# Kernel tuning notes

Measured on AMD Instinct MI355X. Metric: run time of the kernel, lower is better.

## Reference

```python
import jax, jax.numpy as jnp
import numpy as np

N = 50000        # total nodes across batch
K = 16           # max neighbors per node (padded with index 0)
E = 800000       # directed edges / messages
B = 1024         # molecules
MAXM = 48        # max nodes per molecule (padded with index 0)
FEATURE_FDIM = 9
ALL_FDIM = 10    # feature_dist_graph (9) + reshaped rij distance (1)
H = 64           # hidden_dim
NUM_ITERS = 2
NEG_INF = -1e9


def setup_inputs() -> dict:
    key = jax.random.key(0)
    ks = jax.random.split(key, 16)
    s = 1.0 / np.sqrt(H)
    return {
        "target_features": jax.random.normal(ks[0], (N, FEATURE_FDIM), jnp.float32),
        "feature_dist_graph": jax.random.normal(ks[1], (E, ALL_FDIM - 1), jnp.float32),
        "rij_dist_pairs": jax.random.uniform(ks[2], (E,), jnp.float32),
        "start_end_env": jax.random.randint(ks[3], (N, K), 0, N + 1),
        "b_scope": jax.random.randint(ks[4], (N, K), 0, E),
        "l_scope": jax.random.randint(ks[5], (B, MAXM), 0, N + 1),
        "scope_update": jax.random.randint(ks[6], (E,), 0, N + 1),
        "scope_update_lig": jax.random.randint(ks[7], (E,), 0, N + 1),
        "W_emb": jax.random.uniform(ks[8], (FEATURE_FDIM, H), jnp.float32, 0.1, 0.9),
        "b_emb": jnp.zeros((H,), jnp.float32),
        "W_dist": jax.random.uniform(ks[9], (ALL_FDIM, H), jnp.float32, 0.1, 0.9),
        "b_dist": jnp.zeros((H,), jnp.float32),
        "W_gat": jax.random.normal(ks[10], (H, H), jnp.float32) * s,
        "Wm_gat": jax.random.normal(ks[11], (H, H), jnp.float32) * s,
        "a_gat": jax.random.normal(ks[12], (2 * H,), jnp.float32) * s,
    }


def reference(target_features, feature_dist_graph, rij_dist_pairs,
              start_end_env, b_scope, l_scope, scope_update, scope_update_lig,
              W_emb, b_emb, W_dist, b_dist, W_gat, Wm_gat, a_gat):
    # node embedding over origin features
    h = target_features @ W_emb + b_emb                        # [N, H]
    # edge message embedding over pair features + distance
    msg_in = jnp.concatenate([feature_dist_graph, rij_dist_pairs[:, None]], axis=1)
    message = msg_in @ W_dist + b_dist                         # [E, H]
    # prepend zero pad row (index 0 = padding for ragged gathers)
    hp = jnp.concatenate([jnp.zeros((1, H), h.dtype), h], axis=0)  # [N+1, H]
    pad_mask = (start_end_env == 0)                            # [N, K]
    upd_mask = (scope_update_lig > 0).astype(h.dtype)[:, None]  # [E, 1]
    for _ in range(NUM_ITERS):
        nb = hp[start_end_env]                                 # [N, K, H] gather neighbors
        mg = message[b_scope]                                  # [N, K, H] gather messages
        Wn = nb @ W_gat                                        # [N, K, H]
        Wm = mg @ Wm_gat                                       # [N, K, H]
        # GAT attention logits: leaky_relu(a^T [Wn || Wm])
        logits = jax.nn.leaky_relu(
            jnp.einsum('nkh,h->nk', Wn, a_gat[:H]) +
            jnp.einsum('nkh,h->nk', Wm, a_gat[H:]), 0.2)       # [N, K]
        logits = jnp.where(pad_mask, NEG_INF, logits)
        alpha = jax.nn.softmax(logits, axis=1)                 # [N, K]
        new_h = jax.nn.elu(jnp.einsum('nk,nkh->nh', alpha, Wn + Wm))  # [N, H]
        hp = jnp.concatenate([jnp.zeros((1, H), new_h.dtype), new_h], axis=0)
        # scatter updated node features back into edge messages
        message = hp[scope_update] * upd_mask                  # [E, H]
    cmp_enc = hp[l_scope]                                      # [B, MAXM, H]
    return cmp_enc.sum(axis=1)                                 # [B, H]
```

## Files before the change

kernel.cpp:

```cpp
#include <hip/hip_runtime.h>
#include <hip/hip_bf16.h>

#define N_NODES 50000
#define K_NB 16
#define E_EDGES 800000
#define B_MOL 1024
#define MAXM_M 48
#define FDIM 9
#define ADIM 10
#define H 64
#define NEG_INF_F (-1e9f)
#define NODE_BLOCKS 12500
#define EDGE_BLOCKS 3125

__device__ inline float readlane_f(float v, int l) {
    return __int_as_float(__builtin_amdgcn_readlane(__float_as_int(v), l));
}
__device__ inline int readlane_i(int v, int l) {
    return __builtin_amdgcn_readlane(v, l);
}
__device__ inline float bf2f(unsigned u) {
    return __uint_as_float(u << 16);
}
__device__ inline unsigned short f2bf(float f) {
    unsigned x = __float_as_uint(f);
    return (unsigned short)((x + 0x7fffu + ((x >> 16) & 1u)) >> 16);
}

#define GLOAD_U16(dst, voff, sbase) \
    asm volatile("global_load_ushort %0, %1, %2" : "=v"(dst) : "v"(voff), "s"(sbase))
#define GLOAD_F32(dst, voff, sbase) \
    asm volatile("global_load_dword %0, %1, %2" : "=v"(dst) : "v"(voff), "s"(sbase))

__global__ __launch_bounds__(256) void k_fold(
    const float* __restrict__ W_emb, const float* __restrict__ b_emb,
    const float* __restrict__ W_dist, const float* __restrict__ b_dist,
    const float* __restrict__ W_gat, const float* __restrict__ Wm_gat,
    const float* __restrict__ a_gat,
    float* __restrict__ W2, float* __restrict__ c2,
    float* __restrict__ W3, float* __restrict__ c3,
    float* __restrict__ wa, float* __restrict__ ca)
{
    int tid = blockIdx.x * 256 + threadIdx.x;
    if (tid < 640) {
        int j = tid >> 6, h = tid & 63;
        float acc = 0.f;
        for (int t = 0; t < H; ++t) acc += W_dist[j * H + t] * Wm_gat[t * H + h];
        W2[tid] = acc;
    } else if (tid < 704) {
        int h = tid - 640;
        float acc = 0.f;
        for (int t = 0; t < H; ++t) acc += b_dist[t] * Wm_gat[t * H + h];
        c2[h] = acc;
    } else if (tid < 1280) {
        int q = tid - 704, j = q >> 6, h = q & 63;
        float acc = 0.f;
        for (int t = 0; t < H; ++t) acc += W_emb[j * H + t] * W_gat[t * H + h];
        W3[q] = acc;
    } else if (tid < 1344) {
        int h = tid - 1280;
        float acc = 0.f;
        for (int t = 0; t < H; ++t) acc += b_emb[t] * W_gat[t * H + h];
        c3[h] = acc;
    } else if (tid < 1408) {
        int lane = tid - 1344;
        float v = 0.f;
        for (int h = 0; h < H; ++h) v += Wm_gat[lane * H + h] * a_gat[H + h];
        float acc = 0.f;
        for (int t = 0; t < H; ++t) {
            float vt = readlane_f(v, t);
            if (lane < ADIM)       acc += W_dist[lane * H + t] * vt;
            else if (lane == ADIM) acc += b_dist[t] * vt;
        }
        if (lane < ADIM)       wa[lane] = acc;
        else if (lane == ADIM) ca[0] = acc;
    }
}

__global__ __launch_bounds__(256) void k_pre(
    const float* __restrict__ tf, const float* __restrict__ fdg,
    const float* __restrict__ rij,
    const int* __restrict__ su, const int* __restrict__ sul,
    const float* __restrict__ W3, const float* __restrict__ c3,
    const float* __restrict__ wa, const float* __restrict__ ca,
    const float* __restrict__ a_gat,
    unsigned short* __restrict__ WGh16, float* __restrict__ t1,
    unsigned short* __restrict__ emsg, int* __restrict__ sue)
{
    int bid = blockIdx.x;
    if (bid < NODE_BLOCKS) {
        int tid = bid * 256 + threadIdx.x;
        int n = tid >> 6, h = tid & 63;
        if (tid < 64) { WGh16[tid] = 0; if (tid == 0) t1[0] = 0.f; }
        float acc = c3[h];
#pragma unroll
        for (int j = 0; j < FDIM; ++j) acc += tf[n * FDIM + j] * W3[j * H + h];
        WGh16[(size_t)(n + 1) * H + h] = f2bf(acc);
        float tv = acc * a_gat[h];
#pragma unroll
        for (int o = 32; o > 0; o >>= 1) tv += __shfl_xor(tv, o, 64);
        if (h == 0) t1[n + 1] = tv;
    } else {
        int e = (bid - NODE_BLOCKS) * 256 + threadIdx.x;
        float f[ADIM];
#pragma unroll
        for (int j = 0; j < FDIM; ++j) f[j] = fdg[(size_t)e * FDIM + j];
        f[FDIM] = rij[e];
        float acc = ca[0];
#pragma unroll
        for (int j = 0; j < ADIM; ++j) acc += f[j] * wa[j];
        unsigned rec[8];
#pragma unroll
        for (int j = 0; j < 5; ++j)
            rec[j] = (unsigned)f2bf(f[2 * j]) | ((unsigned)f2bf(f[2 * j + 1]) << 16);
        rec[5] = __float_as_uint(acc);
        rec[6] = 0; rec[7] = 0;
        uint4* dst = (uint4*)(emsg + (size_t)e * 16);
        dst[0] = make_uint4(rec[0], rec[1], rec[2], rec[3]);
        dst[1] = make_uint4(rec[4], rec[5], rec[6], rec[7]);
        sue[e] = (sul[e] > 0) ? su[e] : 0;
    }
}

template <int ITER>
__global__ __launch_bounds__(256) void k_gat(
    const int* __restrict__ sse, const int* __restrict__ bsc,
    const unsigned short* __restrict__ WGh16, const float* __restrict__ t1,
    const unsigned short* __restrict__ emsg,
    const float* __restrict__ W2, const float* __restrict__ c2,
    const int* __restrict__ sue, const float* __restrict__ t2,
    const unsigned short* __restrict__ WhWm16,
    float* __restrict__ hp_out)
{
    int wave = threadIdx.x >> 6;
    int lane = threadIdx.x & 63;
    int n = blockIdx.x * 4 + wave;
    if (n == 0) hp_out[lane] = 0.f;
    if (n >= N_NODES) return;

    int kidx = 0, ke = 0, ksu = 0;
    float lg = NEG_INF_F;
    if (lane < K_NB) {
        kidx = sse[n * K_NB + lane];
        ke   = bsc[n * K_NB + lane];
        float g2;
        if (ITER == 1) {
            g2 = __uint_as_float(*(const unsigned*)(emsg + (size_t)ke * 16 + 10));
        } else {
            ksu = sue[ke];
            g2 = t2[ksu];
        }
        float p = t1[kidx] + g2;
        p = (p > 0.f) ? p : 0.2f * p;
        lg = (kidx == 0) ? NEG_INF_F : p;
    }

    unsigned wn_u[K_NB], wm_u[K_NB];
    int off  = lane * 2;
    int offm = (lane & 15) * 2;
#pragma unroll
    for (int k = 0; k < K_NB; ++k) {
        const unsigned short* pk = WGh16 + (size_t)readlane_i(kidx, k) * H;
        GLOAD_U16(wn_u[k], off, pk);
    }
#pragma unroll
    for (int k = 0; k < K_NB; ++k) {
        if (ITER == 1) {
            const unsigned short* pe = emsg + (size_t)readlane_i(ke, k) * 16;
            GLOAD_U16(wm_u[k], offm, pe);
        } else {
            const unsigned short* ps = WhWm16 + (size_t)readlane_i(ksu, k) * H;
            GLOAD_U16(wm_u[k], off, ps);
        }
    }

    float m = lg;
#pragma unroll
    for (int o = 8; o > 0; o >>= 1) m = fmaxf(m, __shfl_xor(m, o, 64));
    float ex = __expf(lg - m);
    float s = ex;
#pragma unroll
    for (int o = 8; o > 0; o >>= 1) s += __shfl_xor(s, o, 64);
    float alpha = ex / s;

    asm volatile("s_waitcnt vmcnt(0)"
        : "+v"(wn_u[0]), "+v"(wn_u[1]), "+v"(wn_u[2]), "+v"(wn_u[3]),
          "+v"(wn_u[4]), "+v"(wn_u[5]), "+v"(wn_u[6]), "+v"(wn_u[7]),
          "+v"(wn_u[8]), "+v"(wn_u[9]), "+v"(wn_u[10]), "+v"(wn_u[11]),
          "+v"(wn_u[12]), "+v"(wn_u[13]), "+v"(wn_u[14]), "+v"(wn_u[15]));
    asm volatile(""
        : "+v"(wm_u[0]), "+v"(wm_u[1]), "+v"(wm_u[2]), "+v"(wm_u[3]),
          "+v"(wm_u[4]), "+v"(wm_u[5]), "+v"(wm_u[6]), "+v"(wm_u[7]),
          "+v"(wm_u[8]), "+v"(wm_u[9]), "+v"(wm_u[10]), "+v"(wm_u[11]),
          "+v"(wm_u[12]), "+v"(wm_u[13]), "+v"(wm_u[14]), "+v"(wm_u[15]));

    float acc = 0.f;
    float fr = 0.f;
#pragma unroll
    for (int k = 0; k < K_NB; ++k) {
        float ak = readlane_f(alpha, k);
        if (ITER == 1) {
            acc += ak * bf2f(wn_u[k]);
            fr  += ak * bf2f(wm_u[k]);
        } else {
            acc += ak * (bf2f(wn_u[k]) + bf2f(wm_u[k]));
        }
    }
    if (ITER == 1) {
        float wmacc = c2[lane];
#pragma unroll
        for (int j = 0; j < ADIM; ++j)
            wmacc += readlane_f(fr, j) * W2[j * H + lane];
        acc += wmacc;
    }
    float o = (acc > 0.f) ? acc : expm1f(acc);
    hp_out[(size_t)(n + 1) * H + lane] = o;
}

__global__ __launch_bounds__(256) void k_gemm2(
    const float* __restrict__ hp,
    const float* __restrict__ W_gat, const float* __restrict__ Wm_gat,
    const float* __restrict__ a_gat,
    unsigned short* __restrict__ WGh16, unsigned short* __restrict__ WhWm16,
    float* __restrict__ t1, float* __restrict__ t2)
{
    int lane = threadIdx.x & 63;
    float wg[H], wm[H];
#pragma unroll
    for (int j = 0; j < H; ++j) {
        wg[j] = W_gat[j * H + lane];
        wm[j] = Wm_gat[j * H + lane];
    }
    float a1 = a_gat[lane], a2 = a_gat[H + lane];
    int row = blockIdx.x * 4 + (threadIdx.x >> 6);
    int stride = gridDim.x * 4;
    for (; row <= N_NODES; row += stride) {
        float hv = hp[(size_t)row * H + lane];
        float a = 0.f, b = 0.f;
#pragma unroll
        for (int j = 0; j < H; ++j) {
            float hj = readlane_f(hv, j);
            a += hj * wg[j];
            b += hj * wm[j];
        }
        WGh16[(size_t)row * H + lane]  = f2bf(a);
        WhWm16[(size_t)row * H + lane] = f2bf(b);
        float ta = a * a1, tb = b * a2;
#pragma unroll
        for (int o = 32; o > 0; o >>= 1) {
            ta += __shfl_xor(ta, o, 64);
            tb += __shfl_xor(tb, o, 64);
        }
        if (lane == 0) { t1[row] = ta; t2[row] = tb; }
    }
}

__global__ __launch_bounds__(256) void k_out(
    const int* __restrict__ l_scope, const float* __restrict__ hp,
    float* __restrict__ out)
{
    int wave = threadIdx.x >> 6;
    int lane = threadIdx.x & 63;
    int b = blockIdx.x * 4 + wave;
    if (b >= B_MOL) return;
    int idx48 = (lane < MAXM_M) ? l_scope[b * MAXM_M + lane] : 0;
    float v[MAXM_M];
    int off = lane * 4;
#pragma unroll
    for (int m = 0; m < MAXM_M; ++m) {
        const float* pm = hp + (size_t)readlane_i(idx48, m) * H;
        GLOAD_F32(v[m], off, pm);
    }
    asm volatile("s_waitcnt vmcnt(0)"
        : "+v"(v[0]), "+v"(v[1]), "+v"(v[2]), "+v"(v[3]),
          "+v"(v[4]), "+v"(v[5]), "+v"(v[6]), "+v"(v[7]),
          "+v"(v[8]), "+v"(v[9]), "+v"(v[10]), "+v"(v[11]),
          "+v"(v[12]), "+v"(v[13]), "+v"(v[14]), "+v"(v[15]));
    asm volatile(""
        : "+v"(v[16]), "+v"(v[17]), "+v"(v[18]), "+v"(v[19]),
          "+v"(v[20]), "+v"(v[21]), "+v"(v[22]), "+v"(v[23]),
          "+v"(v[24]), "+v"(v[25]), "+v"(v[26]), "+v"(v[27]),
          "+v"(v[28]), "+v"(v[29]), "+v"(v[30]), "+v"(v[31]));
    asm volatile(""
        : "+v"(v[32]), "+v"(v[33]), "+v"(v[34]), "+v"(v[35]),
          "+v"(v[36]), "+v"(v[37]), "+v"(v[38]), "+v"(v[39]),
          "+v"(v[40]), "+v"(v[41]), "+v"(v[42]), "+v"(v[43]),
          "+v"(v[44]), "+v"(v[45]), "+v"(v[46]), "+v"(v[47]));
    float acc = 0.f;
#pragma unroll
    for (int m = 0; m < MAXM_M; ++m) acc += v[m];
    out[b * H + lane] = acc;
}

extern "C" void kernel_launch(void* const* d_in, const int* in_sizes, int n_in,
                              void* d_out, int out_size, void* d_ws, size_t ws_size,
                              hipStream_t stream)
{
    const float* tf     = (const float*)d_in[0];
    const float* fdg    = (const float*)d_in[1];
    const float* rij    = (const float*)d_in[2];
    const int*   sse    = (const int*)d_in[3];
    const int*   bsc    = (const int*)d_in[4];
    const int*   lsc    = (const int*)d_in[5];
    const int*   su     = (const int*)d_in[6];
    const int*   sul    = (const int*)d_in[7];
    const float* W_emb  = (const float*)d_in[8];
    const float* b_emb  = (const float*)d_in[9];
    const float* W_dist = (const float*)d_in[10];
    const float* b_dist = (const float*)d_in[11];
    const float* W_gat  = (const float*)d_in[12];
    const float* Wm_gat = (const float*)d_in[13];
    const float* a_gat  = (const float*)d_in[14];
    float* out = (float*)d_out;

    char* base = (char*)d_ws;
    size_t off = 0;
    auto alloc = [&](size_t bytes) {
        char* p = base + off;
        off = (off + bytes + 255) & ~(size_t)255;
        return p;
    };
    float* W2   = (float*)alloc(640 * 4);
    float* c2   = (float*)alloc(64 * 4);
    float* W3   = (float*)alloc(576 * 4);
    float* c3   = (float*)alloc(64 * 4);
    float* wa   = (float*)alloc(16 * 4);
    float* ca   = (float*)alloc(16 * 4);
    float* t1   = (float*)alloc((size_t)(N_NODES + 1) * 4);
    float* t2   = (float*)alloc((size_t)(N_NODES + 1) * 4);
    int*   sue  = (int*)alloc((size_t)E_EDGES * 4);
    unsigned short* WGh16  = (unsigned short*)alloc((size_t)(N_NODES + 1) * H * 2);
    unsigned short* WhWm16 = (unsigned short*)alloc((size_t)(N_NODES + 1) * H * 2);
    float* hp2  = (float*)alloc((size_t)(N_NODES + 1) * H * 4);
    char*  big  = alloc((size_t)E_EDGES * 32);
    unsigned short* emsg = (unsigned short*)big;
    float* hp3  = (float*)big;

    k_fold<<<dim3(6), dim3(256), 0, stream>>>(W_emb, b_emb, W_dist, b_dist,
                                              W_gat, Wm_gat, a_gat,
                                              W2, c2, W3, c3, wa, ca);

    k_pre<<<dim3(NODE_BLOCKS + EDGE_BLOCKS), dim3(256), 0, stream>>>(
        tf, fdg, rij, su, sul, W3, c3, wa, ca, a_gat, WGh16, t1, emsg, sue);

    dim3 gat_grid((N_NODES + 3) / 4);
    k_gat<1><<<gat_grid, dim3(256), 0, stream>>>(
        sse, bsc, WGh16, t1, emsg, W2, c2, sue, t2, WhWm16, hp2);

    k_gemm2<<<dim3(1024), dim3(256), 0, stream>>>(
        hp2, W_gat, Wm_gat, a_gat, WGh16, WhWm16, t1, t2);

    k_gat<2><<<gat_grid, dim3(256), 0, stream>>>(
        sse, bsc, WGh16, t1, emsg, W2, c2, sue, t2, WhWm16, hp3);

    k_out<<<dim3(B_MOL / 4), dim3(256), 0, stream>>>(lsc, hp3, out);
}
```

Baseline: 234.2 us.

## Aggregate raw features before projection and fold the second GEMM into gather kernels

```diff
diff --git a/kernel.cpp b/kernel.cpp
--- a/kernel.cpp
+++ b/kernel.cpp
@@ -10,7 +10,7 @@
 #define ADIM 10
 #define H 64
 #define NEG_INF_F (-1e9f)
-#define NODE_BLOCKS 12500
+#define PRE_NODE_BLOCKS 196
 #define EDGE_BLOCKS 3125
 
 __device__ inline float readlane_f(float v, int l) {
@@ -31,6 +31,19 @@
     asm volatile("global_load_ushort %0, %1, %2" : "=v"(dst) : "v"(voff), "s"(sbase))
 #define GLOAD_F32(dst, voff, sbase) \
     asm volatile("global_load_dword %0, %1, %2" : "=v"(dst) : "v"(voff), "s"(sbase))
+
+#define DRAIN16(a) \
+    asm volatile("s_waitcnt vmcnt(0)" \
+        : "+v"(a[0]), "+v"(a[1]), "+v"(a[2]), "+v"(a[3]), \
+          "+v"(a[4]), "+v"(a[5]), "+v"(a[6]), "+v"(a[7]), \
+          "+v"(a[8]), "+v"(a[9]), "+v"(a[10]), "+v"(a[11]), \
+          "+v"(a[12]), "+v"(a[13]), "+v"(a[14]), "+v"(a[15]))
+#define HOLD16(a) \
+    asm volatile("" \
+        : "+v"(a[0]), "+v"(a[1]), "+v"(a[2]), "+v"(a[3]), \
+          "+v"(a[4]), "+v"(a[5]), "+v"(a[6]), "+v"(a[7]), \
+          "+v"(a[8]), "+v"(a[9]), "+v"(a[10]), "+v"(a[11]), \
+          "+v"(a[12]), "+v"(a[13]), "+v"(a[14]), "+v"(a[15]))
 
 __global__ __launch_bounds__(256) void k_fold(
     const float* __restrict__ W_emb, const float* __restrict__ b_emb,
@@ -39,41 +52,60 @@
     const float* __restrict__ a_gat,
     float* __restrict__ W2, float* __restrict__ c2,
     float* __restrict__ W3, float* __restrict__ c3,
-    float* __restrict__ wa, float* __restrict__ ca)
-{
-    int tid = blockIdx.x * 256 + threadIdx.x;
-    if (tid < 640) {
-        int j = tid >> 6, h = tid & 63;
-        float acc = 0.f;
-        for (int t = 0; t < H; ++t) acc += W_dist[j * H + t] * Wm_gat[t * H + h];
-        W2[tid] = acc;
-    } else if (tid < 704) {
-        int h = tid - 640;
+    float* __restrict__ wa, float* __restrict__ ca,
+    float* __restrict__ va, float* __restrict__ vb,
+    float* __restrict__ wv9, float* __restrict__ cv)
+{
+    __shared__ float s_va[64], s_vb[64];
+    int tid = threadIdx.x;
+    int h = tid & 63, g = tid >> 6;
+    if (g == 0) {
+        float acc = 0.f;
+        for (int t = 0; t < H; ++t) acc += W_gat[h * H + t] * a_gat[t];
+        s_va[h] = acc; va[h] = acc;
+    } else if (g == 1) {
+        float acc = 0.f;
+        for (int t = 0; t < H; ++t) acc += Wm_gat[h * H + t] * a_gat[H + t];
+        s_vb[h] = acc; vb[h] = acc;
+    } else if (g == 2) {
         float acc = 0.f;
         for (int t = 0; t < H; ++t) acc += b_dist[t] * Wm_gat[t * H + h];
         c2[h] = acc;
-    } else if (tid < 1280) {
-        int q = tid - 704, j = q >> 6, h = q & 63;
-        float acc = 0.f;
-        for (int t = 0; t < H; ++t) acc += W_emb[j * H + t] * W_gat[t * H + h];
-        W3[q] = acc;
-    } else if (tid < 1344) {
-        int h = tid - 1280;
+    } else {
         float acc = 0.f;
         for (int t = 0; t < H; ++t) acc += b_emb[t] * W_gat[t * H + h];
         c3[h] = acc;
-    } else if (tid < 1408) {
-        int lane = tid - 1344;
-        float v = 0.f;
-        for (int h = 0; h < H; ++h) v += Wm_gat[lane * H + h] * a_gat[H + h];
-        float acc = 0.f;
-        for (int t = 0; t < H; ++t) {
-            float vt = readlane_f(v, t);
-            if (lane < ADIM)       acc += W_dist[lane * H + t] * vt;
-            else if (lane == ADIM) acc += b_dist[t] * vt;
-        }
-        if (lane < ADIM)       wa[lane] = acc;
-        else if (lane == ADIM) ca[0] = acc;
+    }
+    __syncthreads();
+    for (int q = tid; q < 640; q += 256) {
+        int j = q >> 6, hh = q & 63;
+        float acc = 0.f;
+        for (int t = 0; t < H; ++t) acc += W_dist[j * H + t] * Wm_gat[t * H + hh];
+        W2[q] = acc;
+    }
+    for (int q = tid; q < 576; q += 256) {
+        int j = q >> 6, hh = q & 63;
+        float acc = 0.f;
+        for (int t = 0; t < H; ++t) acc += W_emb[j * H + t] * W_gat[t * H + hh];
+        W3[q] = acc;
+    }
+    if (tid < ADIM) {
+        float acc = 0.f;
+        for (int t = 0; t < H; ++t) acc += W_dist[tid * H + t] * s_vb[t];
+        wa[tid] = acc;
+    } else if (tid == ADIM) {
+        float acc = 0.f;
+        for (int t = 0; t < H; ++t) acc += b_dist[t] * s_vb[t];
+        ca[0] = acc;
+    } else if (tid >= 16 && tid < 16 + FDIM) {
+        int j = tid - 16;
+        float acc = 0.f;
+        for (int t = 0; t < H; ++t) acc += W_emb[j * H + t] * s_va[t];
+        wv9[j] = acc;
+    } else if (tid == 31) {
+        float acc = 0.f;
+        for (int t = 0; t < H; ++t) acc += b_emb[t] * s_va[t];
+        cv[0] = acc;
     }
 }
 
@@ -81,27 +113,39 @@
     const float* __restrict__ tf, const float* __restrict__ fdg,
     const float* __restrict__ rij,
     const int* __restrict__ su, const int* __restrict__ sul,
-    const float* __restrict__ W3, const float* __restrict__ c3,
     const float* __restrict__ wa, const float* __restrict__ ca,
-    const float* __restrict__ a_gat,
-    unsigned short* __restrict__ WGh16, float* __restrict__ t1,
+    const float* __restrict__ wv9, const float* __restrict__ cv,
+    float* __restrict__ t1A, unsigned short* __restrict__ tfp,
     unsigned short* __restrict__ emsg, int* __restrict__ sue)
 {
     int bid = blockIdx.x;
-    if (bid < NODE_BLOCKS) {
-        int tid = bid * 256 + threadIdx.x;
-        int n = tid >> 6, h = tid & 63;
-        if (tid < 64) { WGh16[tid] = 0; if (tid == 0) t1[0] = 0.f; }
-        float acc = c3[h];
-#pragma unroll
-        for (int j = 0; j < FDIM; ++j) acc += tf[n * FDIM + j] * W3[j * H + h];
-        WGh16[(size_t)(n + 1) * H + h] = f2bf(acc);
-        float tv = acc * a_gat[h];
-#pragma unroll
-        for (int o = 32; o > 0; o >>= 1) tv += __shfl_xor(tv, o, 64);
-        if (h == 0) t1[n + 1] = tv;
+    if (bid < PRE_NODE_BLOCKS) {
+        int n = bid * 256 + threadIdx.x;
+        if (n == 0) {
+            t1A[0] = 0.f;
+            uint4 z = make_uint4(0, 0, 0, 0);
+            ((uint4*)tfp)[0] = z; ((uint4*)tfp)[1] = z;
+        }
+        if (n >= N_NODES) return;
+        float f[FDIM];
+        float acc = cv[0];
+#pragma unroll
+        for (int j = 0; j < FDIM; ++j) {
+            f[j] = tf[n * FDIM + j];
+            acc += f[j] * wv9[j];
+        }
+        t1A[n + 1] = acc;
+        unsigned rec[8];
+#pragma unroll
+        for (int j = 0; j < 4; ++j)
+            rec[j] = (unsigned)f2bf(f[2 * j]) | ((unsigned)f2bf(f[2 * j + 1]) << 16);
+        rec[4] = (unsigned)f2bf(f[8]);
+        rec[5] = 0; rec[6] = 0; rec[7] = 0;
+        uint4* dst = (uint4*)(tfp + (size_t)(n + 1) * 16);
+        dst[0] = make_uint4(rec[0], rec[1], rec[2], rec[3]);
+        dst[1] = make_uint4(rec[4], rec[5], rec[6], rec[7]);
     } else {
-        int e = (bid - NODE_BLOCKS) * 256 + threadIdx.x;
+        int e = (bid - PRE_NODE_BLOCKS) * 256 + threadIdx.x;
         float f[ADIM];
 #pragma unroll
         for (int j = 0; j < FDIM; ++j) f[j] = fdg[(size_t)e * FDIM + j];
@@ -122,56 +166,47 @@
     }
 }
 
-template <int ITER>
-__global__ __launch_bounds__(256) void k_gat(
+__global__ __launch_bounds__(256) void k_gat1(
     const int* __restrict__ sse, const int* __restrict__ bsc,
-    const unsigned short* __restrict__ WGh16, const float* __restrict__ t1,
+    const float* __restrict__ t1A, const unsigned short* __restrict__ tfp,
     const unsigned short* __restrict__ emsg,
     const float* __restrict__ W2, const float* __restrict__ c2,
-    const int* __restrict__ sue, const float* __restrict__ t2,
-    const unsigned short* __restrict__ WhWm16,
-    float* __restrict__ hp_out)
+    const float* __restrict__ W3, const float* __restrict__ c3,
+    const float* __restrict__ va, const float* __restrict__ vb,
+    unsigned short* __restrict__ hp2bf, float* __restrict__ t1B,
+    float* __restrict__ t2B)
 {
     int wave = threadIdx.x >> 6;
     int lane = threadIdx.x & 63;
     int n = blockIdx.x * 4 + wave;
-    if (n == 0) hp_out[lane] = 0.f;
+    if (n == 0) {
+        hp2bf[lane] = 0;
+        if (lane == 0) { t1B[0] = 0.f; t2B[0] = 0.f; }
+    }
     if (n >= N_NODES) return;
 
-    int kidx = 0, ke = 0, ksu = 0;
+    int kidx = 0, ke = 0;
     float lg = NEG_INF_F;
     if (lane < K_NB) {
         kidx = sse[n * K_NB + lane];
         ke   = bsc[n * K_NB + lane];
-        float g2;
-        if (ITER == 1) {
-            g2 = __uint_as_float(*(const unsigned*)(emsg + (size_t)ke * 16 + 10));
-        } else {
-            ksu = sue[ke];
-            g2 = t2[ksu];
-        }
-        float p = t1[kidx] + g2;
+        float g2 = __uint_as_float(*(const unsigned*)(emsg + (size_t)ke * 16 + 10));
+        float p = t1A[kidx] + g2;
         p = (p > 0.f) ? p : 0.2f * p;
         lg = (kidx == 0) ? NEG_INF_F : p;
     }
 
     unsigned wn_u[K_NB], wm_u[K_NB];
-    int off  = lane * 2;
-    int offm = (lane & 15) * 2;
-#pragma unroll
-    for (int k = 0; k < K_NB; ++k) {
-        const unsigned short* pk = WGh16 + (size_t)readlane_i(kidx, k) * H;
-        GLOAD_U16(wn_u[k], off, pk);
-    }
-#pragma unroll
-    for (int k = 0; k < K_NB; ++k) {
-        if (ITER == 1) {
-            const unsigned short* pe = emsg + (size_t)readlane_i(ke, k) * 16;
-            GLOAD_U16(wm_u[k], offm, pe);
-        } else {
-            const unsigned short* ps = WhWm16 + (size_t)readlane_i(ksu, k) * H;
-            GLOAD_U16(wm_u[k], off, ps);
-        }
+    int offr = (lane & 15) * 2;
+#pragma unroll
+    for (int k = 0; k < K_NB; ++k) {
+        const unsigned short* pk = tfp + (size_t)readlane_i(kidx, k) * 16;
+        GLOAD_U16(wn_u[k], offr, pk);
+    }
+#pragma unroll
+    for (int k = 0; k < K_NB; ++k) {
+        const unsigned short* pe = emsg + (size_t)readlane_i(ke, k) * 16;
+        GLOAD_U16(wm_u[k], offr, pe);
     }
 
     float m = lg;
@@ -183,76 +218,98 @@
     for (int o = 8; o > 0; o >>= 1) s += __shfl_xor(s, o, 64);
     float alpha = ex / s;
 
-    asm volatile("s_waitcnt vmcnt(0)"
-        : "+v"(wn_u[0]), "+v"(wn_u[1]), "+v"(wn_u[2]), "+v"(wn_u[3]),
-          "+v"(wn_u[4]), "+v"(wn_u[5]), "+v"(wn_u[6]), "+v"(wn_u[7]),
-          "+v"(wn_u[8]), "+v"(wn_u[9]), "+v"(wn_u[10]), "+v"(wn_u[11]),
-          "+v"(wn_u[12]), "+v"(wn_u[13]), "+v"(wn_u[14]), "+v"(wn_u[15]));
-    asm volatile(""
-        : "+v"(wm_u[0]), "+v"(wm_u[1]), "+v"(wm_u[2]), "+v"(wm_u[3]),
-          "+v"(wm_u[4]), "+v"(wm_u[5]), "+v"(wm_u[6]), "+v"(wm_u[7]),
-          "+v"(wm_u[8]), "+v"(wm_u[9]), "+v"(wm_u[10]), "+v"(wm_u[11]),
-          "+v"(wm_u[12]), "+v"(wm_u[13]), "+v"(wm_u[14]), "+v"(wm_u[15]));
-
+    DRAIN16(wn_u);
+    HOLD16(wm_u);
+
+    float fr = 0.f, frm = 0.f, beta = 0.f;
+#pragma unroll
+    for (int k = 0; k < K_NB; ++k) {
+        float ak = readlane_f(alpha, k);
+        fr  += ak * bf2f(wn_u[k]);
+        frm += ak * bf2f(wm_u[k]);
+        beta += (readlane_i(kidx, k) > 0) ? ak : 0.f;
+    }
+    float acc = c2[lane] + beta * c3[lane];
+#pragma unroll
+    for (int j = 0; j < FDIM; ++j) acc += readlane_f(fr, j) * W3[j * H + lane];
+#pragma unroll
+    for (int j = 0; j < ADIM; ++j) acc += readlane_f(frm, j) * W2[j * H + lane];
+    float o = (acc > 0.f) ? acc : expm1f(acc);
+    hp2bf[(size_t)(n + 1) * H + lane] = f2bf(o);
+    float ta = o * va[lane], tb = o * vb[lane];
+#pragma unroll
+    for (int q = 32; q > 0; q >>= 1) {
+        ta += __shfl_xor(ta, q, 64);
+        tb += __shfl_xor(tb, q, 64);
+    }
+    if (lane == 0) { t1B[n + 1] = ta; t2B[n + 1] = tb; }
+}
+
+__global__ __launch_bounds__(256) void k_gat2(
+    const int* __restrict__ sse, const int* __restrict__ bsc,
+    const int* __restrict__ sue,
+    const float* __restrict__ t1B, const float* __restrict__ t2B,
+    const unsigned short* __restrict__ hp2bf,
+    const float* __restrict__ W_gat, const float* __restrict__ Wm_gat,
+    float* __restrict__ hp3)
+{
+    int wave = threadIdx.x >> 6;
+    int lane = threadIdx.x & 63;
+    int n = blockIdx.x * 4 + wave;
+    if (n == 0) hp3[lane] = 0.f;
+    if (n >= N_NODES) return;
+
+    int kidx = 0, ksu = 0;
+    float lg = NEG_INF_F;
+    if (lane < K_NB) {
+        kidx = sse[n * K_NB + lane];
+        int ke = bsc[n * K_NB + lane];
+        ksu = sue[ke];
+        float p = t1B[kidx] + t2B[ksu];
+        p = (p > 0.f) ? p : 0.2f * p;
+        lg = (kidx == 0) ? NEG_INF_F : p;
+    }
+
+    unsigned wn_u[K_NB], wm_u[K_NB];
+    int off = lane * 2;
+#pragma unroll
+    for (int k = 0; k < K_NB; ++k) {
+        const unsigned short* pk = hp2bf + (size_t)readlane_i(kidx, k) * H;
+        GLOAD_U16(wn_u[k], off, pk);
+    }
+#pragma unroll
+    for (int k = 0; k < K_NB; ++k) {
+        const unsigned short* ps = hp2bf + (size_t)readlane_i(ksu, k) * H;
+        GLOAD_U16(wm_u[k], off, ps);
+    }
+
+    float m = lg;
+#pragma unroll
+    for (int o = 8; o > 0; o >>= 1) m = fmaxf(m, __shfl_xor(m, o, 64));
+    float ex = __expf(lg - m);
+    float s = ex;
+#pragma unroll
+    for (int o = 8; o > 0; o >>= 1) s += __shfl_xor(s, o, 64);
+    float alpha = ex / s;
+
+    DRAIN16(wn_u);
+    HOLD16(wm_u);
+
+    float gn = 0.f, gm = 0.f;
+#pragma unroll
+    for (int k = 0; k < K_NB; ++k) {
+        float ak = readlane_f(alpha, k);
+        gn += ak * bf2f(wn_u[k]);
+        gm += ak * bf2f(wm_u[k]);
+    }
     float acc = 0.f;
-    float fr = 0.f;
-#pragma unroll
-    for (int k = 0; k < K_NB; ++k) {
-        float ak = readlane_f(alpha, k);
-        if (ITER == 1) {
-            acc += ak * bf2f(wn_u[k]);
-            fr  += ak * bf2f(wm_u[k]);
-        } else {
-            acc += ak * (bf2f(wn_u[k]) + bf2f(wm_u[k]));
-        }
-    }
-    if (ITER == 1) {
-        float wmacc = c2[lane];
-#pragma unroll
-        for (int j = 0; j < ADIM; ++j)
-            wmacc += readlane_f(fr, j) * W2[j * H + lane];
-        acc += wmacc;
+#pragma unroll
+    for (int j = 0; j < H; ++j) {
+        acc += readlane_f(gn, j) * W_gat[j * H + lane];
+        acc += readlane_f(gm, j) * Wm_gat[j * H + lane];
     }
     float o = (acc > 0.f) ? acc : expm1f(acc);
-    hp_out[(size_t)(n + 1) * H + lane] = o;
-}
-
-__global__ __launch_bounds__(256) void k_gemm2(
-    const float* __restrict__ hp,
-    const float* __restrict__ W_gat, const float* __restrict__ Wm_gat,
-    const float* __restrict__ a_gat,
-    unsigned short* __restrict__ WGh16, unsigned short* __restrict__ WhWm16,
-    float* __restrict__ t1, float* __restrict__ t2)
-{
-    int lane = threadIdx.x & 63;
-    float wg[H], wm[H];
-#pragma unroll
-    for (int j = 0; j < H; ++j) {
-        wg[j] = W_gat[j * H + lane];
-        wm[j] = Wm_gat[j * H + lane];
-    }
-    float a1 = a_gat[lane], a2 = a_gat[H + lane];
-    int row = blockIdx.x * 4 + (threadIdx.x >> 6);
-    int stride = gridDim.x * 4;
-    for (; row <= N_NODES; row += stride) {
-        float hv = hp[(size_t)row * H + lane];
-        float a = 0.f, b = 0.f;
-#pragma unroll
-        for (int j = 0; j < H; ++j) {
-            float hj = readlane_f(hv, j);
-            a += hj * wg[j];
-            b += hj * wm[j];
-        }
-        WGh16[(size_t)row * H + lane]  = f2bf(a);
-        WhWm16[(size_t)row * H + lane] = f2bf(b);
-        float ta = a * a1, tb = b * a2;
-#pragma unroll
-        for (int o = 32; o > 0; o >>= 1) {
-            ta += __shfl_xor(ta, o, 64);
-            tb += __shfl_xor(tb, o, 64);
-        }
-        if (lane == 0) { t1[row] = ta; t2[row] = tb; }
-    }
+    hp3[(size_t)(n + 1) * H + lane] = o;
 }
 
 __global__ __launch_bounds__(256) void k_out(
@@ -322,36 +379,37 @@
     };
     float* W2   = (float*)alloc(640 * 4);
     float* c2   = (float*)alloc(64 * 4);
-    float* W3   = (float*)alloc(576 * 4);
+    float* W3   = (float*)alloc(640 * 4);
     float* c3   = (float*)alloc(64 * 4);
     float* wa   = (float*)alloc(16 * 4);
     float* ca   = (float*)alloc(16 * 4);
-    float* t1   = (float*)alloc((size_t)(N_NODES + 1) * 4);
-    float* t2   = (float*)alloc((size_t)(N_NODES + 1) * 4);
+    float* va   = (float*)alloc(64 * 4);
+    float* vb   = (float*)alloc(64 * 4);
+    float* wv9  = (float*)alloc(16 * 4);
+    float* cv   = (float*)alloc(16 * 4);
+    float* t1A  = (float*)alloc((size_t)(N_NODES + 1) * 4);
+    float* t1B  = (float*)alloc((size_t)(N_NODES + 1) * 4);
+    float* t2B  = (float*)alloc((size_t)(N_NODES + 1) * 4);
     int*   sue  = (int*)alloc((size_t)E_EDGES * 4);
-    unsigned short* WGh16  = (unsigned short*)alloc((size_t)(N_NODES + 1) * H * 2);
-    unsigned short* WhWm16 = (unsigned short*)alloc((size_t)(N_NODES + 1) * H * 2);
-    float* hp2  = (float*)alloc((size_t)(N_NODES + 1) * H * 4);
-    char*  big  = alloc((size_t)E_EDGES * 32);
+    unsigned short* tfp   = (unsigned short*)alloc((size_t)(N_NODES + 1) * 16 * 2);
+    unsigned short* hp2bf = (unsigned short*)alloc((size_t)(N_NODES + 1) * H * 2);
+    char* big = alloc((size_t)E_EDGES * 32);
     unsigned short* emsg = (unsigned short*)big;
-    float* hp3  = (float*)big;
-
-    k_fold<<<dim3(6), dim3(256), 0, stream>>>(W_emb, b_emb, W_dist, b_dist,
-                                              W_gat, Wm_gat, a_gat,
-                                              W2, c2, W3, c3, wa, ca);
-
-    k_pre<<<dim3(NODE_BLOCKS + EDGE_BLOCKS), dim3(256), 0, stream>>>(
-        tf, fdg, rij, su, sul, W3, c3, wa, ca, a_gat, WGh16, t1, emsg, sue);
+    float* hp3 = (float*)big;
+
+    k_fold<<<dim3(1), dim3(256), 0, stream>>>(
+        W_emb, b_emb, W_dist, b_dist, W_gat, Wm_gat, a_gat,
+        W2, c2, W3, c3, wa, ca, va, vb, wv9, cv);
+
+    k_pre<<<dim3(PRE_NODE_BLOCKS + EDGE_BLOCKS), dim3(256), 0, stream>>>(
+        tf, fdg, rij, su, sul, wa, ca, wv9, cv, t1A, tfp, emsg, sue);
 
     dim3 gat_grid((N_NODES + 3) / 4);
-    k_gat<1><<<gat_grid, dim3(256), 0, stream>>>(
-        sse, bsc, WGh16, t1, emsg, W2, c2, sue, t2, WhWm16, hp2);
-
-    k_gemm2<<<dim3(1024), dim3(256), 0, stream>>>(
-        hp2, W_gat, Wm_gat, a_gat, WGh16, WhWm16, t1, t2);
-
-    k_gat<2><<<gat_grid, dim3(256), 0, stream>>>(
-        sse, bsc, WGh16, t1, emsg, W2, c2, sue, t2, WhWm16, hp3);
+    k_gat1<<<gat_grid, dim3(256), 0, stream>>>(
+        sse, bsc, t1A, tfp, emsg, W2, c2, W3, c3, va, vb, hp2bf, t1B, t2B);
+
+    k_gat2<<<gat_grid, dim3(256), 0, stream>>>(
+        sse, bsc, sue, t1B, t2B, hp2bf, W_gat, Wm_gat, hp3);
 
     k_out<<<dim3(B_MOL / 4), dim3(256), 0, stream>>>(lsc, hp3, out);
 }
```

New measurement: 233.0 us. No clear change (-0.5%).
